# Optimization experiments

Hardware: AMD Instinct MI355X
Metric: run time of the kernel (lower is better)

## Reference

```python
import jax, jax.numpy as jnp
import numpy as np

B, S, DIN, DIM, H = 2, 2304, 1024, 1024, 16
HEAD_DIM = DIM // H            # 64
ROT_DIM = HEAD_DIM             # partial_rotary_factor = 1
BASE = 10000.0
EPS = 1e-6


def setup_inputs() -> dict:
    key = jax.random.key(0)
    ks = jax.random.split(key, 6)
    return {
        "input": jax.random.normal(ks[0], (B, S, DIN), dtype=jnp.float32),
        "qkv_w": jax.random.normal(ks[1], (3 * DIM, DIN), dtype=jnp.float32) * 0.02,
        "qkv_b": jnp.zeros((3 * DIM,), dtype=jnp.float32),
        "q_scale": jnp.ones((DIM,), dtype=jnp.float32),
        "k_scale": jnp.ones((DIM,), dtype=jnp.float32),
        "proj_w": jax.random.normal(ks[2], (DIN, DIM), dtype=jnp.float32) * 0.02,
        "proj_b": jnp.zeros((DIN,), dtype=jnp.float32),
        "height": 48,
        "width": 48,
    }


def _rms_norm(x, scale):
    # RMSNorm over the full inner dim (QKNorm), learned scale
    var = jnp.mean(x * x, axis=-1, keepdims=True)
    return x * jax.lax.rsqrt(var + EPS) * scale


def _rope_1d(x, pos):
    # x: (b, n, h, d_ax), pos: (n,) float; rotate_half-style RoPE
    d = x.shape[-1]
    inv_freq = 1.0 / (BASE ** (jnp.arange(0, d, 2, dtype=jnp.float32) / d))  # (d/2,)
    ang = pos[:, None] * inv_freq                                            # (n, d/2)
    cos = jnp.concatenate([jnp.cos(ang), jnp.cos(ang)], axis=-1)[None, :, None, :]
    sin = jnp.concatenate([jnp.sin(ang), jnp.sin(ang)], axis=-1)[None, :, None, :]
    x1, x2 = jnp.split(x, 2, axis=-1)
    rot = jnp.concatenate([-x2, x1], axis=-1)
    return x * cos + rot * sin


def _rope_2d(x, height, width):
    # axial 2D RoPE: first half of rotary dims keyed by row, second half by col
    n = height * width
    idx = jnp.arange(n, dtype=jnp.float32)
    rows = jnp.floor(idx / width)
    cols = jnp.mod(idx, width)
    half = ROT_DIM // 2
    x_r = _rope_1d(x[..., :half], rows)
    x_c = _rope_1d(x[..., half:ROT_DIM], cols)
    return jnp.concatenate([x_r, x_c, x[..., ROT_DIM:]], axis=-1)


def reference(input, qkv_w, qkv_b, q_scale, k_scale, proj_w, proj_b, height, width):
    b, n, _ = input.shape
    qkv = input @ qkv_w.T + qkv_b                       # (b, n, 3*dim)
    q, k, v = jnp.split(qkv, 3, axis=-1)
    q = _rms_norm(q, q_scale)
    k = _rms_norm(k, k_scale)
    # (b, n, h, d)
    q = q.reshape(b, n, H, HEAD_DIM)
    k = k.reshape(b, n, H, HEAD_DIM)
    v = v.reshape(b, n, H, HEAD_DIM)
    q = _rope_2d(q, height, width)
    k = _rope_2d(k, height, width)
    scale = HEAD_DIM ** (-0.5)
    # (b, h, q, k)
    scores = jnp.einsum("bqhd,bkhd->bhqk", q, k) * scale
    attn = jax.nn.softmax(scores, axis=-1)
    out = jnp.einsum("bhqk,bkhd->bqhd", attn, v)        # (b, n, h, d)
    out = out.reshape(b, n, DIM)
    return out @ proj_w.T + proj_b
```

## Files before the change

kernel.cpp:

```cpp
#include <hip/hip_runtime.h>
#include <math.h>

#define BB   2
#define SS   2304
#define DINC 1024
#define DIMC 1024
#define HH   16
#define HD   64

typedef _Float16 half_t;
typedef __attribute__((ext_vector_type(4))) _Float16 half4;
typedef __attribute__((ext_vector_type(8))) _Float16 half8;
typedef __attribute__((ext_vector_type(4))) float    f32x4;

#define LOG2E 1.44269504088896340736f
#define EXP2(x) __builtin_amdgcn_exp2f(x)

__device__ __forceinline__ half4 lo4(half8 x) { return (half4){x[0], x[1], x[2], x[3]}; }
__device__ __forceinline__ half4 hi4(half8 x) { return (half4){x[4], x[5], x[6], x[7]}; }

#define GLOAD_LDS16(gp, lp)                                                     \
    __builtin_amdgcn_global_load_lds(                                           \
        (const __attribute__((address_space(1))) void*)(gp),                    \
        (__attribute__((address_space(3))) void*)(lp), 16, 0, 0)

template<int RB>
__global__ __launch_bounds__(256)
void convert_tile_f16(const float* __restrict__ src, half_t* __restrict__ dst, int K)
{
    constexpr int EPT = RB * 32 / 256;
    const int mb = blockIdx.x;
    const int kb = blockIdx.y;
    const int t  = threadIdx.x;
    const int e0 = t * EPT;
    const int mm = e0 >> 5;
    const int kk = e0 & 31;
    const float* sp = src + (size_t)(mb * RB + mm) * K + kb * 32 + kk;
    half_t*      dp = dst + ((size_t)mb * (K >> 5) + kb) * (RB * 32) + mm * 32 + kk;
    #pragma unroll
    for (int g = 0; g < EPT / 4; ++g) {
        float4 v = *(const float4*)(sp + 4 * g);
        dp[4 * g + 0] = (half_t)v.x; dp[4 * g + 1] = (half_t)v.y;
        dp[4 * g + 2] = (half_t)v.z; dp[4 * g + 3] = (half_t)v.w;
    }
}

template<int BN, bool OUT_HALF>
__global__ __launch_bounds__(256)
void gemm_mfma(const half_t* __restrict__ Ah, const half_t* __restrict__ Bh,
               const float* __restrict__ bias, void* __restrict__ Cout,
               int M, int N, int K)
{
    constexpr int MT = (BN == 128) ? 4 : 2;
    constexpr int NT = 4;
    const int KB = K >> 5;
    __shared__ half_t As[8192];
    __shared__ half_t Bs[2 * BN * 32];

    const int t    = threadIdx.x;
    const int w    = t >> 6;
    const int lane = t & 63;
    const int l15  = lane & 15, quad = lane >> 4;
    const int wr   = (BN == 128) ? (w >> 1) : w;
    const int wc   = (BN == 128) ? (w & 1) : 0;
    const int mb   = blockIdx.y, nb = blockIdx.x;

    f32x4 acc[MT][NT];
    #pragma unroll
    for (int mt = 0; mt < MT; ++mt)
        #pragma unroll
        for (int nt = 0; nt < NT; ++nt) acc[mt][nt] = (f32x4){0.f, 0.f, 0.f, 0.f};

    const half_t* atile = Ah + (size_t)mb * KB * 4096;
    const half_t* btile = Bh + (size_t)nb * KB * (BN * 32);

    for (int kb = 0; kb < KB; kb += 2) {
        #pragma unroll
        for (int u = 0; u < 2; ++u) {
            const half_t* at = atile + (size_t)(kb + u) * 4096;
            const half_t* bt = btile + (size_t)(kb + u) * (BN * 32);
            #pragma unroll
            for (int v = 0; v < 2; ++v) {
                const int ch = w * 2 + v;
                GLOAD_LDS16(at + ch * 512 + lane * 8, As + u * 4096 + ch * 512);
            }
            if (BN == 128) {
                #pragma unroll
                for (int v = 0; v < 2; ++v) {
                    const int ch = w * 2 + v;
                    GLOAD_LDS16(bt + ch * 512 + lane * 8, Bs + u * 4096 + ch * 512);
                }
            } else {
                GLOAD_LDS16(bt + w * 512 + lane * 8, Bs + u * (BN * 32) + w * 512);
            }
        }
        __syncthreads();

        #pragma unroll
        for (int u = 0; u < 2; ++u) {
            half8 af[MT], bf[NT];
            #pragma unroll
            for (int mt = 0; mt < MT; ++mt)
                af[mt] = *(const half8*)(As + u * 4096
                                         + (wr * (MT * 16) + mt * 16 + l15) * 32 + quad * 8);
            #pragma unroll
            for (int nt = 0; nt < NT; ++nt)
                bf[nt] = *(const half8*)(Bs + u * (BN * 32)
                                         + (wc * 64 + nt * 16 + l15) * 32 + quad * 8);
            #pragma unroll
            for (int mt = 0; mt < MT; ++mt)
                #pragma unroll
                for (int nt = 0; nt < NT; ++nt)
                    acc[mt][nt] = __builtin_amdgcn_mfma_f32_16x16x32_f16(
                        af[mt], bf[nt], acc[mt][nt], 0, 0, 0);
        }
        __syncthreads();
    }

    const int bm = mb * 128, bn = nb * BN;
    #pragma unroll
    for (int nt = 0; nt < NT; ++nt) {
        const int n  = bn + wc * 64 + nt * 16 + l15;
        const float bv = bias[n];
        #pragma unroll
        for (int mt = 0; mt < MT; ++mt) {
            const int m0 = bm + wr * (MT * 16) + mt * 16 + quad * 4;
            #pragma unroll
            for (int rg = 0; rg < 4; ++rg) {
                const float v = acc[mt][nt][rg] + bv;
                if (OUT_HALF) ((half_t*)Cout)[(size_t)(m0 + rg) * N + n] = (half_t)v;
                else          ((float*) Cout)[(size_t)(m0 + rg) * N + n] = v;
            }
        }
    }
}

__global__ __launch_bounds__(256)
void normrope_v6(half_t* __restrict__ qkvh, const float* __restrict__ q_scale,
                 const float* __restrict__ k_scale, const int* __restrict__ wptr,
                 half_t* __restrict__ Kf, half_t* __restrict__ Vf)
{
    const int token = blockIdx.x;
    const int s     = token % SS;
    const int b     = token / SS;
    const int w     = *wptr;
    const int t     = threadIdx.x;
    const float rowp = (float)(s / w);
    const float colp = (float)(s % w);

    half_t* base = qkvh + (size_t)token * 3072;

    const int fr = s >> 5;
    const int jt = (s >> 4) & 1;

    {
        half4 v4 = *(const half4*)(base + 2048 + 4 * t);
        const int dabs0 = 4 * t;
        const int h  = dabs0 >> 6;
        const int vq = (s & 15) >> 2;
        const int vi = s & 3;
        half_t* vdst = Vf + ((size_t)(b * HH + h) * 72 + fr) * 2048 + jt * 1024;
        #pragma unroll
        for (int ii = 0; ii < 4; ++ii) {
            const int d   = (dabs0 + ii) & 63;
            const int dt  = d >> 4;
            vdst[(size_t)(dt >> 1) * 512 + ((d & 15) + 16 * vq) * 8 + (dt & 1) * 4 + vi]
                = v4[ii];
        }
    }

    __shared__ float buf[DIMC];
    __shared__ float red[4];

    const int km = s & 15;

    #pragma unroll
    for (int sel = 0; sel < 2; ++sel) {
        half_t* row = base + sel * DIMC;
        const float* scp = sel ? k_scale : q_scale;

        half4 xh = *(const half4*)(row + 4 * t);
        float x0 = (float)xh[0], x1 = (float)xh[1], x2 = (float)xh[2], x3 = (float)xh[3];
        float ss = x0 * x0 + x1 * x1 + x2 * x2 + x3 * x3;
        #pragma unroll
        for (int o = 32; o >= 1; o >>= 1) ss += __shfl_xor(ss, o);
        if ((t & 63) == 0) red[t >> 6] = ss;
        __syncthreads();

        const float rinv = rsqrtf((red[0] + red[1] + red[2] + red[3]) * (1.0f / DIMC) + 1e-6f);
        float4 g = *(const float4*)(scp + 4 * t);
        buf[4 * t + 0] = x0 * rinv * g.x;
        buf[4 * t + 1] = x1 * rinv * g.y;
        buf[4 * t + 2] = x2 * rinv * g.z;
        buf[4 * t + 3] = x3 * rinv * g.w;
        __syncthreads();

        const float qsc = sel ? 1.0f : (0.125f * LOG2E);

        #pragma unroll
        for (int pp = 0; pp < 2; ++pp) {
            const int p = t + pp * 256;
            const int h = p >> 5;
            const int r = p & 31;
            const int j = r & 15;
            const float pos = (r < 16) ? rowp : colp;
            const int d1 = (r < 16) ? j : (32 + j);
            const int d2 = d1 + 16;
            const float freq = exp2f((float)j * -0.83048202372f);
            const float ang  = pos * freq;
            float sn, cs;
            __sincosf(ang, &sn, &cs);
            const float a1 = buf[h * HD + d1], a2 = buf[h * HD + d2];
            const float o1 = (a1 * cs - a2 * sn) * qsc;
            const float o2 = (a2 * cs + a1 * sn) * qsc;
            if (sel == 0) {
                row[h * HD + d1] = (half_t)o1;
                row[h * HD + d2] = (half_t)o2;
            } else {
                half_t* kdst = Kf + ((size_t)(b * HH + h) * 72 + fr) * 2048 + jt * 1024;
                kdst[(size_t)(d1 >> 5) * 512 + (km + 16 * ((d1 & 31) >> 3)) * 8 + (d1 & 7)]
                    = (half_t)o1;
                kdst[(size_t)(d2 >> 5) * 512 + (km + 16 * ((d2 & 31) >> 3)) * 8 + (d2 & 7)]
                    = (half_t)o2;
            }
        }
        __syncthreads();
    }
}

__global__ __launch_bounds__(256, 4)
void flash_attn_mfma8(const half_t* __restrict__ qkvh, const half_t* __restrict__ Kf,
                      const half_t* __restrict__ Vf, half_t* __restrict__ attn_h)
{
    const int flat = blockIdx.x;
    const int xcd  = flat & 7;
    const int jj   = flat >> 3;
    const int bh   = xcd * 4 + (jj / 36);
    const int qtb  = jj % 36;
    const int b    = bh >> 4, h = bh & 15;
    const int t    = threadIdx.x;
    const int w    = t >> 6;
    const int jt   = w & 1;
    const int qh   = w >> 1;
    const int lane = t & 63;
    const int l15  = lane & 15, quad = lane >> 4;

    const size_t tb = (size_t)b * SS;
    const int q0 = qtb * 64;

    __shared__ float mlb[4][32][2];
    __shared__ float Ob[2][64][33];

    half8 qf[2][2];
    #pragma unroll
    for (int qt = 0; qt < 2; ++qt)
        #pragma unroll
        for (int dt2 = 0; dt2 < 2; ++dt2)
            qf[qt][dt2] = *(const half8*)(qkvh + (tb + q0 + qh * 32 + qt * 16 + l15) * 3072
                                          + h * HD + dt2 * 32 + quad * 8);

    f32x4 acc[4][2];
    float m_i[2], l_i[2];
    #pragma unroll
    for (int qt = 0; qt < 2; ++qt) {
        m_i[qt] = -INFINITY; l_i[qt] = 0.f;
        #pragma unroll
        for (int dt = 0; dt < 4; ++dt) acc[dt][qt] = (f32x4){0.f, 0.f, 0.f, 0.f};
    }

    const half_t* kpl = Kf + (size_t)bh * 72 * 2048 + jt * 1024 + lane * 8;
    const half_t* vpl = Vf + (size_t)bh * 72 * 2048 + jt * 1024 + lane * 8;

    half8 kA0 = *(const half8*)(kpl);
    half8 kA1 = *(const half8*)(kpl + 512);
    half8 kB0 = *(const half8*)(kpl + 2048);
    half8 kB1 = *(const half8*)(kpl + 2560);
    half8 vA0 = *(const half8*)(vpl);
    half8 vA1 = *(const half8*)(vpl + 512);
    half8 vB0 = *(const half8*)(vpl + 2048);
    half8 vB1 = *(const half8*)(vpl + 2560);

    for (int p = 0; p < 36; ++p) {
        f32x4 scA[2], scB[2];
        #pragma unroll
        for (int qt = 0; qt < 2; ++qt) {
            scA[qt] = (f32x4){0.f, 0.f, 0.f, 0.f};
            scA[qt] = __builtin_amdgcn_mfma_f32_16x16x32_f16(kA0, qf[qt][0], scA[qt], 0, 0, 0);
            scA[qt] = __builtin_amdgcn_mfma_f32_16x16x32_f16(kA1, qf[qt][1], scA[qt], 0, 0, 0);
            scB[qt] = (f32x4){0.f, 0.f, 0.f, 0.f};
            scB[qt] = __builtin_amdgcn_mfma_f32_16x16x32_f16(kB0, qf[qt][0], scB[qt], 0, 0, 0);
            scB[qt] = __builtin_amdgcn_mfma_f32_16x16x32_f16(kB1, qf[qt][1], scB[qt], 0, 0, 0);
        }

        if (p + 1 < 36) {
            const half_t* kN = kpl + (size_t)(p + 1) * 4096;
            kA0 = *(const half8*)(kN);
            kA1 = *(const half8*)(kN + 512);
            kB0 = *(const half8*)(kN + 2048);
            kB1 = *(const half8*)(kN + 2560);
        }

        half4 pfA[2], pfB[2];
        #pragma unroll
        for (int qt = 0; qt < 2; ++qt) {
            float mx = fmaxf(fmaxf(fmaxf(scA[qt][0], scA[qt][1]),
                                   fmaxf(scA[qt][2], scA[qt][3])),
                             fmaxf(fmaxf(scB[qt][0], scB[qt][1]),
                                   fmaxf(scB[qt][2], scB[qt][3])));
            mx = fmaxf(mx, __shfl_xor(mx, 16));
            mx = fmaxf(mx, __shfl_xor(mx, 32));
            if (__any(mx > m_i[qt])) {
                const float mn = fmaxf(m_i[qt], mx);
                const float alpha = EXP2(m_i[qt] - mn);
                m_i[qt] = mn;
                l_i[qt] *= alpha;
                #pragma unroll
                for (int dt = 0; dt < 4; ++dt) acc[dt][qt] *= alpha;
            }
            const float m = m_i[qt];
            const float a0 = EXP2(scA[qt][0] - m);
            const float a1 = EXP2(scA[qt][1] - m);
            const float a2 = EXP2(scA[qt][2] - m);
            const float a3 = EXP2(scA[qt][3] - m);
            const float b0 = EXP2(scB[qt][0] - m);
            const float b1 = EXP2(scB[qt][1] - m);
            const float b2 = EXP2(scB[qt][2] - m);
            const float b3 = EXP2(scB[qt][3] - m);
            l_i[qt] += ((a0 + a1) + (a2 + a3)) + ((b0 + b1) + (b2 + b3));
            pfA[qt] = (half4){(half_t)a0, (half_t)a1, (half_t)a2, (half_t)a3};
            pfB[qt] = (half4){(half_t)b0, (half_t)b1, (half_t)b2, (half_t)b3};
        }

        half4 vfA[4] = {lo4(vA0), hi4(vA0), lo4(vA1), hi4(vA1)};
        half4 vfB[4] = {lo4(vB0), hi4(vB0), lo4(vB1), hi4(vB1)};
        #pragma unroll
        for (int dt = 0; dt < 4; ++dt)
            #pragma unroll
            for (int qt = 0; qt < 2; ++qt) {
                acc[dt][qt] = __builtin_amdgcn_mfma_f32_16x16x16f16(
                    vfA[dt], pfA[qt], acc[dt][qt], 0, 0, 0);
                acc[dt][qt] = __builtin_amdgcn_mfma_f32_16x16x16f16(
                    vfB[dt], pfB[qt], acc[dt][qt], 0, 0, 0);
            }

        if (p + 1 < 36) {
            const half_t* vN = vpl + (size_t)(p + 1) * 4096;
            vA0 = *(const half8*)(vN);
            vA1 = *(const half8*)(vN + 512);
            vB0 = *(const half8*)(vN + 2048);
            vB1 = *(const half8*)(vN + 2560);
        }
    }

    #pragma unroll
    for (int qt = 0; qt < 2; ++qt) {
        float lq = l_i[qt];
        lq += __shfl_xor(lq, 16);
        lq += __shfl_xor(lq, 32);
        if (quad == 0) {
            mlb[w][qt * 16 + l15][0] = m_i[qt];
            mlb[w][qt * 16 + l15][1] = lq;
        }
    }
    __syncthreads();

    float fac[2];
    #pragma unroll
    for (int qt = 0; qt < 2; ++qt) {
        const int q = qt * 16 + l15;
        const float m0 = mlb[qh * 2 + 0][q][0], m1 = mlb[qh * 2 + 1][q][0];
        const float M  = fmaxf(m0, m1);
        const float L  = mlb[qh * 2 + 0][q][1] * EXP2(m0 - M)
                       + mlb[qh * 2 + 1][q][1] * EXP2(m1 - M);
        fac[qt] = EXP2(m_i[qt] - M) / L;
    }

    #pragma unroll
    for (int ph = 0; ph < 2; ++ph) {
        if (jt == ph) {
            #pragma unroll
            for (int dt = 0; dt < 4; ++dt)
                #pragma unroll
                for (int qt = 0; qt < 2; ++qt)
                    #pragma unroll
                    for (int rg = 0; rg < 4; ++rg) {
                        const int d = dt * 16 + quad * 4 + rg;
                        const int q = qt * 16 + l15;
                        const float v = acc[dt][qt][rg] * fac[qt];
                        if (ph == 0) Ob[qh][d][q] = v;
                        else         Ob[qh][d][q] += v;
                    }
        }
        __syncthreads();
    }

    {
        const int q   = t >> 2;
        const int ds  = (t & 3) * 16;
        const int qh2 = q >> 5, qq = q & 31;
        const size_t mrow = tb + q0 + q;
        const int mb2 = (int)(mrow >> 7);
        const int mm  = (int)(mrow & 127);
        #pragma unroll
        for (int g = 0; g < 4; ++g) {
            const int dd = ds + 4 * g;
            const int kb2 = (h * HD + dd) >> 5;
            const int kk  = dd & 31;
            half4 o;
            o[0] = (half_t)Ob[qh2][dd + 0][qq];
            o[1] = (half_t)Ob[qh2][dd + 1][qq];
            o[2] = (half_t)Ob[qh2][dd + 2][qq];
            o[3] = (half_t)Ob[qh2][dd + 3][qq];
            *(half4*)(attn_h + ((size_t)mb2 * 32 + kb2) * 4096 + mm * 32 + kk) = o;
        }
    }
}

extern "C" void kernel_launch(void* const* d_in, const int* in_sizes, int n_in,
                              void* d_out, int out_size, void* d_ws, size_t ws_size,
                              hipStream_t stream)
{
    const float* input   = (const float*)d_in[0];
    const float* qkv_w   = (const float*)d_in[1];
    const float* qkv_b   = (const float*)d_in[2];
    const float* q_scale = (const float*)d_in[3];
    const float* k_scale = (const float*)d_in[4];
    const float* proj_w  = (const float*)d_in[5];
    const float* proj_b  = (const float*)d_in[6];
    const int*   width   = (const int*)d_in[8];
    float* out = (float*)d_out;

    half_t* qkvh   = (half_t*)d_ws;
    half_t* attn_h = qkvh   + (size_t)4608 * 3072;
    half_t* Vf     = attn_h + (size_t)4608 * 1024;
    half_t* Ah     = Vf     + (size_t)32 * 72 * 2048;
    half_t* Bh1    = Ah     + (size_t)4608 * 1024;
    half_t* Bh2    = Bh1    + (size_t)3072 * 1024;
    half_t* Kf     = Ah;

    const int M = BB * SS;

    convert_tile_f16<128><<<dim3(M / 128, DINC / 32),        256, 0, stream>>>(input,  Ah,  DINC);
    convert_tile_f16<128><<<dim3(3 * DIMC / 128, DINC / 32), 256, 0, stream>>>(qkv_w, Bh1, DINC);
    convert_tile_f16<64><<<dim3(DINC / 64, DIMC / 32),       256, 0, stream>>>(proj_w, Bh2, DIMC);

    gemm_mfma<128, true><<<dim3(3 * DIMC / 128, M / 128), 256, 0, stream>>>(
        Ah, Bh1, qkv_b, qkvh, M, 3 * DIMC, DINC);

    normrope_v6<<<M, 256, 0, stream>>>(qkvh, q_scale, k_scale, width, Kf, Vf);

    flash_attn_mfma8<<<dim3(SS / 64 * BB * HH), 256, 0, stream>>>(qkvh, Kf, Vf, attn_h);

    gemm_mfma<64, false><<<dim3(DINC / 64, M / 128), 256, 0, stream>>>(
        attn_h, Bh2, proj_b, out, M, DINC, DIMC);
}
```

Before: 265.2 us.

## Repack K/V layout for 16x16x32 PV MFMA and split attention into 32-query blocks

Changes the K and V fragment layout written by the norm/rope kernel so that the P·V product uses the 16x16x32 f16 MFMA instead of pairs of 16x16x16 MFMAs. The attention kernel drops to 128 threads covering 32 queries per block, with each wave handling one key half, and launches twice as many blocks. It also adds a lazy rescale threshold that only updates the running max when it grows by more than 8, to skip rescaling work. Costs are more redundant K/V streaming across blocks and a possible fp16 overflow risk in P when the stale max is kept.

```diff
diff --git a/kernel.cpp b/kernel.cpp
--- a/kernel.cpp
+++ b/kernel.cpp
@@ -15,9 +15,6 @@
 
 #define LOG2E 1.44269504088896340736f
 #define EXP2(x) __builtin_amdgcn_exp2f(x)
-
-__device__ __forceinline__ half4 lo4(half8 x) { return (half4){x[0], x[1], x[2], x[3]}; }
-__device__ __forceinline__ half4 hi4(half8 x) { return (half4){x[4], x[5], x[6], x[7]}; }
 
 #define GLOAD_LDS16(gp, lp)                                                     \
     __builtin_amdgcn_global_load_lds(                                           \
@@ -136,7 +133,7 @@
 }
 
 __global__ __launch_bounds__(256)
-void normrope_v6(half_t* __restrict__ qkvh, const float* __restrict__ q_scale,
+void normrope_v7(half_t* __restrict__ qkvh, const float* __restrict__ q_scale,
                  const float* __restrict__ k_scale, const int* __restrict__ wptr,
                  half_t* __restrict__ Kf, half_t* __restrict__ Vf)
 {
@@ -150,29 +147,26 @@
 
     half_t* base = qkvh + (size_t)token * 3072;
 
-    const int fr = s >> 5;
-    const int jt = (s >> 4) & 1;
+    const int c    = s >> 5;
+    const int slot = s & 31;
+    const int ktile = (slot >> 2) & 1;
+    const int krow  = ((slot >> 3) << 2) + (slot & 3);
 
     {
         half4 v4 = *(const half4*)(base + 2048 + 4 * t);
         const int dabs0 = 4 * t;
         const int h  = dabs0 >> 6;
-        const int vq = (s & 15) >> 2;
-        const int vi = s & 3;
-        half_t* vdst = Vf + ((size_t)(b * HH + h) * 72 + fr) * 2048 + jt * 1024;
+        const int sl3 = slot >> 3, sl7 = slot & 7;
+        half_t* vdst = Vf + ((size_t)(b * HH + h) * 72 + c) * 2048;
         #pragma unroll
         for (int ii = 0; ii < 4; ++ii) {
-            const int d   = (dabs0 + ii) & 63;
-            const int dt  = d >> 4;
-            vdst[(size_t)(dt >> 1) * 512 + ((d & 15) + 16 * vq) * 8 + (dt & 1) * 4 + vi]
-                = v4[ii];
+            const int d = (dabs0 + ii) & 63;
+            vdst[(d >> 4) * 512 + (sl3 * 16 + (d & 15)) * 8 + sl7] = v4[ii];
         }
     }
 
     __shared__ float buf[DIMC];
     __shared__ float red[4];
-
-    const int km = s & 15;
 
     #pragma unroll
     for (int sel = 0; sel < 2; ++sel) {
@@ -217,47 +211,45 @@
                 row[h * HD + d1] = (half_t)o1;
                 row[h * HD + d2] = (half_t)o2;
             } else {
-                half_t* kdst = Kf + ((size_t)(b * HH + h) * 72 + fr) * 2048 + jt * 1024;
-                kdst[(size_t)(d1 >> 5) * 512 + (km + 16 * ((d1 & 31) >> 3)) * 8 + (d1 & 7)]
-                    = (half_t)o1;
-                kdst[(size_t)(d2 >> 5) * 512 + (km + 16 * ((d2 & 31) >> 3)) * 8 + (d2 & 7)]
-                    = (half_t)o2;
+                half_t* kdst = Kf + ((size_t)(b * HH + h) * 72 + c) * 2048;
+                kdst[((ktile << 1) + (d1 >> 5)) * 512
+                     + ((((d1 & 31) >> 3) << 4) + krow) * 8 + (d1 & 7)] = (half_t)o1;
+                kdst[((ktile << 1) + (d2 >> 5)) * 512
+                     + ((((d2 & 31) >> 3) << 4) + krow) * 8 + (d2 & 7)] = (half_t)o2;
             }
         }
         __syncthreads();
     }
 }
 
-__global__ __launch_bounds__(256, 4)
-void flash_attn_mfma8(const half_t* __restrict__ qkvh, const half_t* __restrict__ Kf,
+__global__ __launch_bounds__(128, 4)
+void flash_attn_mfma9(const half_t* __restrict__ qkvh, const half_t* __restrict__ Kf,
                       const half_t* __restrict__ Vf, half_t* __restrict__ attn_h)
 {
     const int flat = blockIdx.x;
     const int xcd  = flat & 7;
-    const int jj   = flat >> 3;
-    const int bh   = xcd * 4 + (jj / 36);
-    const int qtb  = jj % 36;
+    const int idx  = flat >> 3;
+    const int bh   = xcd * 4 + idx / 72;
+    const int qtb  = idx % 72;
     const int b    = bh >> 4, h = bh & 15;
     const int t    = threadIdx.x;
-    const int w    = t >> 6;
-    const int jt   = w & 1;
-    const int qh   = w >> 1;
+    const int jt   = t >> 6;
     const int lane = t & 63;
     const int l15  = lane & 15, quad = lane >> 4;
 
     const size_t tb = (size_t)b * SS;
-    const int q0 = qtb * 64;
-
-    __shared__ float mlb[4][32][2];
-    __shared__ float Ob[2][64][33];
+    const int q0 = qtb * 32;
+
+    __shared__ float mlb[2][32][2];
+    __shared__ float Ob[64][33];
 
     half8 qf[2][2];
     #pragma unroll
     for (int qt = 0; qt < 2; ++qt)
         #pragma unroll
-        for (int dt2 = 0; dt2 < 2; ++dt2)
-            qf[qt][dt2] = *(const half8*)(qkvh + (tb + q0 + qh * 32 + qt * 16 + l15) * 3072
-                                          + h * HD + dt2 * 32 + quad * 8);
+        for (int dg = 0; dg < 2; ++dg)
+            qf[qt][dg] = *(const half8*)(qkvh + (tb + q0 + qt * 16 + l15) * 3072
+                                          + h * HD + dg * 32 + quad * 8);
 
     f32x4 acc[4][2];
     float m_i[2], l_i[2];
@@ -268,39 +260,39 @@
         for (int dt = 0; dt < 4; ++dt) acc[dt][qt] = (f32x4){0.f, 0.f, 0.f, 0.f};
     }
 
-    const half_t* kpl = Kf + (size_t)bh * 72 * 2048 + jt * 1024 + lane * 8;
-    const half_t* vpl = Vf + (size_t)bh * 72 * 2048 + jt * 1024 + lane * 8;
-
-    half8 kA0 = *(const half8*)(kpl);
-    half8 kA1 = *(const half8*)(kpl + 512);
-    half8 kB0 = *(const half8*)(kpl + 2048);
-    half8 kB1 = *(const half8*)(kpl + 2560);
-    half8 vA0 = *(const half8*)(vpl);
-    half8 vA1 = *(const half8*)(vpl + 512);
-    half8 vB0 = *(const half8*)(vpl + 2048);
-    half8 vB1 = *(const half8*)(vpl + 2560);
+    const half_t* kpl = Kf + (size_t)bh * 147456 + jt * 2048 + lane * 8;
+    const half_t* vpl = Vf + (size_t)bh * 147456 + jt * 2048 + lane * 8;
+
+    half8 k00 = *(const half8*)(kpl);
+    half8 k01 = *(const half8*)(kpl + 512);
+    half8 k10 = *(const half8*)(kpl + 1024);
+    half8 k11 = *(const half8*)(kpl + 1536);
+    half8 v0  = *(const half8*)(vpl);
+    half8 v1  = *(const half8*)(vpl + 512);
+    half8 v2  = *(const half8*)(vpl + 1024);
+    half8 v3  = *(const half8*)(vpl + 1536);
 
     for (int p = 0; p < 36; ++p) {
         f32x4 scA[2], scB[2];
         #pragma unroll
         for (int qt = 0; qt < 2; ++qt) {
             scA[qt] = (f32x4){0.f, 0.f, 0.f, 0.f};
-            scA[qt] = __builtin_amdgcn_mfma_f32_16x16x32_f16(kA0, qf[qt][0], scA[qt], 0, 0, 0);
-            scA[qt] = __builtin_amdgcn_mfma_f32_16x16x32_f16(kA1, qf[qt][1], scA[qt], 0, 0, 0);
+            scA[qt] = __builtin_amdgcn_mfma_f32_16x16x32_f16(k00, qf[qt][0], scA[qt], 0, 0, 0);
+            scA[qt] = __builtin_amdgcn_mfma_f32_16x16x32_f16(k01, qf[qt][1], scA[qt], 0, 0, 0);
             scB[qt] = (f32x4){0.f, 0.f, 0.f, 0.f};
-            scB[qt] = __builtin_amdgcn_mfma_f32_16x16x32_f16(kB0, qf[qt][0], scB[qt], 0, 0, 0);
-            scB[qt] = __builtin_amdgcn_mfma_f32_16x16x32_f16(kB1, qf[qt][1], scB[qt], 0, 0, 0);
+            scB[qt] = __builtin_amdgcn_mfma_f32_16x16x32_f16(k10, qf[qt][0], scB[qt], 0, 0, 0);
+            scB[qt] = __builtin_amdgcn_mfma_f32_16x16x32_f16(k11, qf[qt][1], scB[qt], 0, 0, 0);
         }
 
         if (p + 1 < 36) {
             const half_t* kN = kpl + (size_t)(p + 1) * 4096;
-            kA0 = *(const half8*)(kN);
-            kA1 = *(const half8*)(kN + 512);
-            kB0 = *(const half8*)(kN + 2048);
-            kB1 = *(const half8*)(kN + 2560);
-        }
-
-        half4 pfA[2], pfB[2];
+            k00 = *(const half8*)(kN);
+            k01 = *(const half8*)(kN + 512);
+            k10 = *(const half8*)(kN + 1024);
+            k11 = *(const half8*)(kN + 1536);
+        }
+
+        half8 pf[2];
         #pragma unroll
         for (int qt = 0; qt < 2; ++qt) {
             float mx = fmaxf(fmaxf(fmaxf(scA[qt][0], scA[qt][1]),
@@ -309,7 +301,7 @@
                                    fmaxf(scB[qt][2], scB[qt][3])));
             mx = fmaxf(mx, __shfl_xor(mx, 16));
             mx = fmaxf(mx, __shfl_xor(mx, 32));
-            if (__any(mx > m_i[qt])) {
+            if (__any(mx > m_i[qt] + 8.f)) {
                 const float mn = fmaxf(m_i[qt], mx);
                 const float alpha = EXP2(m_i[qt] - mn);
                 m_i[qt] = mn;
@@ -327,28 +319,25 @@
             const float b2 = EXP2(scB[qt][2] - m);
             const float b3 = EXP2(scB[qt][3] - m);
             l_i[qt] += ((a0 + a1) + (a2 + a3)) + ((b0 + b1) + (b2 + b3));
-            pfA[qt] = (half4){(half_t)a0, (half_t)a1, (half_t)a2, (half_t)a3};
-            pfB[qt] = (half4){(half_t)b0, (half_t)b1, (half_t)b2, (half_t)b3};
-        }
-
-        half4 vfA[4] = {lo4(vA0), hi4(vA0), lo4(vA1), hi4(vA1)};
-        half4 vfB[4] = {lo4(vB0), hi4(vB0), lo4(vB1), hi4(vB1)};
-        #pragma unroll
-        for (int dt = 0; dt < 4; ++dt)
-            #pragma unroll
-            for (int qt = 0; qt < 2; ++qt) {
-                acc[dt][qt] = __builtin_amdgcn_mfma_f32_16x16x16f16(
-                    vfA[dt], pfA[qt], acc[dt][qt], 0, 0, 0);
-                acc[dt][qt] = __builtin_amdgcn_mfma_f32_16x16x16f16(
-                    vfB[dt], pfB[qt], acc[dt][qt], 0, 0, 0);
-            }
+            pf[qt] = (half8){(half_t)a0, (half_t)a1, (half_t)a2, (half_t)a3,
+                             (half_t)b0, (half_t)b1, (half_t)b2, (half_t)b3};
+        }
+
+        #pragma unroll
+        for (int dt = 0; dt < 4; ++dt) {
+            const half8 vf = (dt == 0) ? v0 : (dt == 1) ? v1 : (dt == 2) ? v2 : v3;
+            #pragma unroll
+            for (int qt = 0; qt < 2; ++qt)
+                acc[dt][qt] = __builtin_amdgcn_mfma_f32_16x16x32_f16(
+                    vf, pf[qt], acc[dt][qt], 0, 0, 0);
+        }
 
         if (p + 1 < 36) {
             const half_t* vN = vpl + (size_t)(p + 1) * 4096;
-            vA0 = *(const half8*)(vN);
-            vA1 = *(const half8*)(vN + 512);
-            vB0 = *(const half8*)(vN + 2048);
-            vB1 = *(const half8*)(vN + 2560);
+            v0 = *(const half8*)(vN);
+            v1 = *(const half8*)(vN + 512);
+            v2 = *(const half8*)(vN + 1024);
+            v3 = *(const half8*)(vN + 1536);
         }
     }
 
@@ -358,8 +347,8 @@
         lq += __shfl_xor(lq, 16);
         lq += __shfl_xor(lq, 32);
         if (quad == 0) {
-            mlb[w][qt * 16 + l15][0] = m_i[qt];
-            mlb[w][qt * 16 + l15][1] = lq;
+            mlb[jt][qt * 16 + l15][0] = m_i[qt];
+            mlb[jt][qt * 16 + l15][1] = lq;
         }
     }
     __syncthreads();
@@ -368,10 +357,10 @@
     #pragma unroll
     for (int qt = 0; qt < 2; ++qt) {
         const int q = qt * 16 + l15;
-        const float m0 = mlb[qh * 2 + 0][q][0], m1 = mlb[qh * 2 + 1][q][0];
+        const float m0 = mlb[0][q][0], m1 = mlb[1][q][0];
         const float M  = fmaxf(m0, m1);
-        const float L  = mlb[qh * 2 + 0][q][1] * EXP2(m0 - M)
-                       + mlb[qh * 2 + 1][q][1] * EXP2(m1 - M);
+        const float L  = mlb[0][q][1] * EXP2(m0 - M)
+                       + mlb[1][q][1] * EXP2(m1 - M);
         fac[qt] = EXP2(m_i[qt] - M) / L;
     }
 
@@ -387,8 +376,8 @@
                         const int d = dt * 16 + quad * 4 + rg;
                         const int q = qt * 16 + l15;
                         const float v = acc[dt][qt][rg] * fac[qt];
-                        if (ph == 0) Ob[qh][d][q] = v;
-                        else         Ob[qh][d][q] += v;
+                        if (ph == 0) Ob[d][q] = v;
+                        else         Ob[d][q] += v;
                     }
         }
         __syncthreads();
@@ -397,7 +386,6 @@
     {
         const int q   = t >> 2;
         const int ds  = (t & 3) * 16;
-        const int qh2 = q >> 5, qq = q & 31;
         const size_t mrow = tb + q0 + q;
         const int mb2 = (int)(mrow >> 7);
         const int mm  = (int)(mrow & 127);
@@ -407,10 +395,10 @@
             const int kb2 = (h * HD + dd) >> 5;
             const int kk  = dd & 31;
             half4 o;
-            o[0] = (half_t)Ob[qh2][dd + 0][qq];
-            o[1] = (half_t)Ob[qh2][dd + 1][qq];
-            o[2] = (half_t)Ob[qh2][dd + 2][qq];
-            o[3] = (half_t)Ob[qh2][dd + 3][qq];
+            o[0] = (half_t)Ob[dd + 0][q];
+            o[1] = (half_t)Ob[dd + 1][q];
+            o[2] = (half_t)Ob[dd + 2][q];
+            o[3] = (half_t)Ob[dd + 3][q];
             *(half4*)(attn_h + ((size_t)mb2 * 32 + kb2) * 4096 + mm * 32 + kk) = o;
         }
     }
@@ -447,9 +435,9 @@
     gemm_mfma<128, true><<<dim3(3 * DIMC / 128, M / 128), 256, 0, stream>>>(
         Ah, Bh1, qkv_b, qkvh, M, 3 * DIMC, DINC);
 
-    normrope_v6<<<M, 256, 0, stream>>>(qkvh, q_scale, k_scale, width, Kf, Vf);
-
-    flash_attn_mfma8<<<dim3(SS / 64 * BB * HH), 256, 0, stream>>>(qkvh, Kf, Vf, attn_h);
+    normrope_v7<<<M, 256, 0, stream>>>(qkvh, q_scale, k_scale, width, Kf, Vf);
+
+    flash_attn_mfma9<<<dim3(2304), 128, 0, stream>>>(qkvh, Kf, Vf, attn_h);
 
     gemm_mfma<64, false><<<dim3(DINC / 64, M / 128), 256, 0, stream>>>(
         attn_h, Bh2, proj_b, out, M, DINC, DIMC);
```

Measured after the change: 264.4 us. About the same (-0.3%).
